# Kernel optimization log

Hardware: AMD Instinct MI355X
Metric: run time of the kernel (lower is better)

The kernel has to match this reference:

```python
import jax, jax.numpy as jnp
import numpy as np

N_NODES = 10000
N_EDGES = 160000
MUL = 128          # channel multiplicity
N_SPECIES = 10
SH_OFF = [0, 1, 4, 9, 16]   # spherical-harmonic offsets for l=0..3 (2l+1 each)
RADIAL_IN = 8
SIN_DIM = 32
MAX_DENSITY = 100.0


def setup_inputs() -> dict:
    key = jax.random.key(0)
    ks = jax.random.split(key, 16)
    inp = {
        'node_attrs': jax.random.normal(ks[0], (N_NODES, N_SPECIES), jnp.float32),
        'node_feats': jax.random.normal(ks[1], (N_NODES, MUL), jnp.float32),
        'edge_attrs': jax.random.normal(ks[2], (N_EDGES, 16), jnp.float32),
        'edge_feats': jax.random.normal(ks[3], (N_EDGES, RADIAL_IN), jnp.float32),
        'edge_index': jax.random.randint(ks[4], (2, N_EDGES), 0, N_NODES, jnp.int64),
        'W_up': jax.random.normal(ks[5], (MUL, MUL), jnp.float32),
        'Wr1': jax.random.normal(ks[6], (RADIAL_IN, 64), jnp.float32),
        'Wr2': jax.random.normal(ks[7], (64, 64), jnp.float32),
        'Wr3': jax.random.normal(ks[8], (64, 64), jnp.float32),
        'Wr4': jax.random.normal(ks[9], (64, 4 * MUL), jnp.float32),
        'Wd': jax.random.normal(ks[10], (RADIAL_IN, 1), jnp.float32),
        'Wsin': jax.random.normal(ks[11], (SIN_DIM, MUL), jnp.float32),
        'Wlin': jax.random.normal(ks[12], (4, MUL, MUL), jnp.float32),
        'Wskip': jax.random.normal(ks[13], (4, MUL, N_SPECIES, MUL), jnp.float32),
    }
    return inp


def _sinusoidal_embedding(x):
    # continuous sinusoidal embedding: dim=32, max_density=100
    half = SIN_DIM // 2
    freqs = jnp.exp(-jnp.log(MAX_DENSITY) * jnp.arange(half, dtype=x.dtype) / half)
    ang = x[:, None] * freqs[None, :]          # [N, 16]
    return jnp.concatenate([jnp.sin(ang), jnp.cos(ang)], axis=-1)  # [N, 32]


def reference(node_attrs, node_feats, edge_attrs, edge_feats, edge_index,
              W_up, Wr1, Wr2, Wr3, Wr4, Wd, Wsin, Wlin, Wskip):
    N = node_feats.shape[0]
    sender, receiver = edge_index[0], edge_index[1]

    # linear_up (e3nn o3.Linear on 128x0e, fan-in normalized)
    x = node_feats @ (W_up / np.float32(np.sqrt(MUL)))          # [N, 128]

    # radial MLP: FullyConnectedNet([8,64,64,64,512], silu), fan-in normalized
    h = edge_feats
    for W in (Wr1, Wr2, Wr3):
        h = jax.nn.silu(h @ (W / np.float32(np.sqrt(W.shape[0]))))
    tp_w = (h @ (Wr4 / np.float32(np.sqrt(64)))).reshape(-1, 4, MUL)  # [E, 4, 128]

    # equivariant TP: scalar node feats (x) gathered by sender, uvu path per SH l
    xs = x[sender]                                              # [E, 128]
    weighted = xs[:, None, :] * tp_w                            # [E, 4, 128]
    blocks = []
    for l in range(4):
        sh_l = edge_attrs[:, SH_OFF[l]:SH_OFF[l + 1]]           # [E, 2l+1]
        blk = weighted[:, l, :, None] * sh_l[:, None, :]        # [E, 128, 2l+1]
        blocks.append(blk.reshape(blk.shape[0], -1))
    mji = jnp.concatenate(blocks, axis=-1)                      # [E, 2048]

    # per-edge density gate
    density = jnp.tanh((edge_feats @ Wd) ** 2)                  # [E, 1]

    # scatter-sum messages and density to receivers
    message = jax.ops.segment_sum(mji, receiver, num_segments=N)        # [N, 2048]
    rho = jax.ops.segment_sum(density, receiver, num_segments=N)       # [N, 1]
    message = message / (rho + 1.0)

    # density embedding injected into the l=0 block
    demb = _sinusoidal_embedding(rho[:, 0]) @ Wsin              # [N, 128]
    message = message.at[:, :MUL].add(demb)

    # per-l linear (irreps_mid -> irreps_out), skip_tp with node_attrs, reshape
    out_blocks = []
    for l in range(4):
        d = 2 * l + 1
        blk = message[:, MUL * SH_OFF[l]:MUL * SH_OFF[l + 1]].reshape(N, MUL, d)
        blk = jnp.einsum('nuk,uv->nvk', blk, Wlin[l]) / np.float32(np.sqrt(MUL))
        blk = jnp.einsum('nvk,na,vaw->nwk', blk, node_attrs, Wskip[l]) \
              / np.float32(np.sqrt(MUL * N_SPECIES))
        out_blocks.append(blk)
    return jnp.concatenate(out_blocks, axis=-1)                 # [N, 128, 16]
```

## Files before the change

kernel.cpp:

```cpp
#include <hip/hip_runtime.h>
#include <hip/hip_bf16.h>

#define N_NODES 10000
#define N_EDGES 160000

typedef _Float16 h8 __attribute__((ext_vector_type(8)));
typedef _Float16 h4 __attribute__((ext_vector_type(4)));
typedef float f32x4 __attribute__((ext_vector_type(4)));

__device__ __forceinline__ float silu_f(float v){ return v / (1.f + expf(-v)); }

__global__ __launch_bounds__(256) void k_pre(const float* __restrict__ Wr2,
                                             const float* __restrict__ Wr3,
                                             const float* __restrict__ Wr4,
                                             const float* __restrict__ Wup,
                                             const float* __restrict__ Wlin,
                                             const float* __restrict__ Wskip,
                                             const int* __restrict__ eidx,
                                             _Float16* __restrict__ Wr2T,
                                             _Float16* __restrict__ Wr3T,
                                             _Float16* __restrict__ Wr4T,
                                             _Float16* __restrict__ WupT,
                                             _Float16* __restrict__ WC16T,
                                             int* __restrict__ cnt){
  const int b = blockIdx.x;
  __shared__ float wl[128];
  if (b < 224){
    const int idx = b*256 + threadIdx.x;
    if (idx < 4096){
      const int n = idx >> 6, k = idx & 63;
      Wr2T[idx] = (_Float16)(Wr2[k*64 + n] * 0.125f);
    } else if (idx < 8192){
      const int j = idx - 4096;
      const int n = j >> 6, k = j & 63;
      Wr3T[j] = (_Float16)(Wr3[k*64 + n] * 0.125f);
    } else if (idx < 40960){
      const int j = idx - 8192;
      const int n = j >> 6, k = j & 63;
      Wr4T[j] = (_Float16)(Wr4[k*512 + n] * 0.125f);
    } else if (idx < 57344){
      const int j = idx - 40960;
      const int u = j >> 7, k = j & 127;
      WupT[j] = (_Float16)(Wup[k*128 + u] * 0.08838834764831843f);
    }
  } else if (b < 736){
    const int lu = b - 224;
    const int l  = lu >> 7, u = lu & 127;
    if (threadIdx.x < 128) wl[threadIdx.x] = Wlin[lu*128 + threadIdx.x];
    __syncthreads();
    const float* Wsk = Wskip + (size_t)l * 163840;
    for (int i = threadIdx.x; i < 1280; i += 256){
      float acc = 0.f;
      #pragma unroll 16
      for (int v = 0; v < 128; ++v) acc += wl[v] * Wsk[v*1280 + i];
      const int a = i >> 7, w = i & 127;
      WC16T[((size_t)l*128 + w)*1280 + a*128 + u] =
          (_Float16)(acc * 0.0024705294220065465f);
    }
  } else {
    const int e = (b - 736)*256 + threadIdx.x;
    if (e < N_EDGES) atomicAdd(&cnt[eidx[N_EDGES + e]], 1);
  }
}

__global__ __launch_bounds__(256) void k_scan(const int* __restrict__ cnt,
                                              int* __restrict__ off,
                                              int* __restrict__ cur){
  __shared__ int sums[256];
  const int t = threadIdx.x;
  const int base = t * 40;
  int s = 0;
  for (int i = 0; i < 40; ++i){
    const int idx = base + i;
    if (idx < N_NODES) s += cnt[idx];
  }
  sums[t] = s;
  __syncthreads();
  for (int st = 1; st < 256; st <<= 1){
    const int v = (t >= st) ? sums[t - st] : 0;
    __syncthreads();
    sums[t] += v;
    __syncthreads();
  }
  int pre = (t > 0) ? sums[t - 1] : 0;
  for (int i = 0; i < 40; ++i){
    const int idx = base + i;
    if (idx < N_NODES){
      off[idx] = pre; cur[idx] = pre;
      pre += cnt[idx];
    }
  }
  if (t == 255) off[N_NODES] = sums[255];
}

__global__ __launch_bounds__(256) void k_mid(const int* __restrict__ eidx,
                                             int* __restrict__ cur,
                                             int* __restrict__ elist,
                                             int* __restrict__ esnd,
                                             const float* __restrict__ nf,
                                             const _Float16* __restrict__ WupT,
                                             float* __restrict__ x){
  const int b = blockIdx.x;
  const int tid = threadIdx.x;
  alignas(16) __shared__ _Float16 s_nf[64*128];
  alignas(16) __shared__ _Float16 s_wt[128*128];

  if (b < 625){
    const int e = b * 256 + tid;
    if (e < N_EDGES){
      const int pos = atomicAdd(&cur[eidx[N_EDGES + e]], 1);
      elist[pos] = e;
      esnd[pos]  = eidx[e];
    }
    return;
  }

  const int n0 = (b - 625) * 64;
  {
    const int rl = tid >> 2, part = tid & 3;
    const int gr = n0 + rl;
    #pragma unroll
    for (int j = 0; j < 4; ++j){
      const int cu = part*4 + j;
      h8 hv = (h8){};
      if (gr < N_NODES){
        const float4 v0 = *(const float4*)(nf + (size_t)gr*128 + cu*8);
        const float4 v1 = *(const float4*)(nf + (size_t)gr*128 + cu*8 + 4);
        hv[0]=(_Float16)v0.x; hv[1]=(_Float16)v0.y; hv[2]=(_Float16)v0.z; hv[3]=(_Float16)v0.w;
        hv[4]=(_Float16)v1.x; hv[5]=(_Float16)v1.y; hv[6]=(_Float16)v1.z; hv[7]=(_Float16)v1.w;
      }
      const int cs = (cu & 8) | ((cu & 7) ^ (rl & 7));
      *(h8*)&s_nf[rl*128 + cs*8] = hv;
    }
  }
  {
    const int rl = tid >> 1, part = tid & 1;
    #pragma unroll
    for (int j = 0; j < 8; ++j){
      const int cu = part*8 + j;
      const h8 v = *(const h8*)&WupT[(size_t)rl*128 + cu*8];
      const int cs = (cu & 8) | ((cu & 7) ^ (rl & 7));
      *(h8*)&s_wt[rl*128 + cs*8] = v;
    }
  }
  __syncthreads();

  const int wid = tid >> 6, lane = tid & 63;
  const int li = lane & 15, kg = lane >> 4;

  f32x4 acc[8];
  #pragma unroll
  for (int i = 0; i < 8; ++i) acc[i] = (f32x4){0,0,0,0};

  const int row = wid*16 + li;
  #pragma unroll
  for (int s = 0; s < 4; ++s){
    const int ca = s*4 + kg;
    const int csA = (ca & 8) | ((ca & 7) ^ (row & 7));
    const h8 af = *(const h8*)&s_nf[row*128 + csA*8];
    #pragma unroll
    for (int nt = 0; nt < 8; ++nt){
      const int u = nt*16 + li;
      const int csB = (ca & 8) | ((ca & 7) ^ (u & 7));
      const h8 bf = *(const h8*)&s_wt[u*128 + csB*8];
      acc[nt] = __builtin_amdgcn_mfma_f32_16x16x32_f16(af, bf, acc[nt], 0, 0, 0);
    }
  }
  #pragma unroll
  for (int nt = 0; nt < 8; ++nt){
    #pragma unroll
    for (int r = 0; r < 4; ++r){
      const int gr = n0 + wid*16 + kg*4 + r;
      if (gr < N_NODES) x[(size_t)gr*128 + nt*16 + li] = acc[nt][r];
    }
  }
}

__global__ __launch_bounds__(256) void k_fused(const float* __restrict__ ef,
                                               const float* __restrict__ ea,
                                               const float* __restrict__ x,
                                               const float* __restrict__ Wr1,
                                               const float* __restrict__ Wd,
                                               const _Float16* __restrict__ Wr2T,
                                               const _Float16* __restrict__ Wr3T,
                                               const _Float16* __restrict__ Wr4T,
                                               const float* __restrict__ Wsin,
                                               const int* __restrict__ off,
                                               const int* __restrict__ elist,
                                               const int* __restrict__ esnd,
                                               _Float16* __restrict__ msg16){
  const int n0 = blockIdx.x * 4;
  const int tid = threadIdx.x;
  const int lane = tid & 63, wid = tid >> 6;
  const int li = lane & 15, kg = lane >> 4;
  const int u = tid & 127, h = tid >> 7;

  __shared__ int   s_eid[32];
  __shared__ float s_ef[32][8];
  __shared__ float s_w1[8][64];
  alignas(16) __shared__ _Float16 s_xs[32][136];
  alignas(16) __shared__ _Float16 s_actA[32][64];
  alignas(16) __shared__ _Float16 s_actB[32][64];
  alignas(16) __shared__ _Float16 s_w2[32][520];
  alignas(16) __shared__ float s_sh[32][16];
  __shared__ float s_dd[32];
  __shared__ float s_rho[4];
  __shared__ int   s_offs[5];
  __shared__ float s_emb[4][32];

  if (tid < 5) s_offs[tid] = off[n0 + tid];
  if (tid < 4) s_rho[tid] = 0.f;
  for (int j = tid; j < 512; j += 256) s_w1[j >> 6][j & 63] = Wr1[j];
  __syncthreads();

  const int beg = s_offs[0], end = s_offs[4];
  const int ngrp = (end - beg + 31) >> 5;

  float a0[8] = {0,0,0,0,0,0,0,0};
  float a1[8] = {0,0,0,0,0,0,0,0};
  float a2[8] = {0,0,0,0,0,0,0,0};
  float a3[8] = {0,0,0,0,0,0,0,0};

  for (int grp = 0; grp < ngrp; ++grp){
    const int pbase = beg + grp*32;

    if (tid < 32) s_eid[tid] = (pbase + tid < end) ? elist[pbase + tid] : -1;
    __syncthreads();

    {
      const int e = tid >> 3, i = tid & 7;
      const int eid = s_eid[e];
      s_ef[e][i] = (eid >= 0) ? ef[(size_t)eid*8 + i] : 0.f;
    }
    {
      const int e = tid >> 3, qq = tid & 7;
      const int p = pbase + e;
      const int snd = (p < end) ? esnd[p] : 0;
      const float4* xp = (const float4*)(x + (size_t)snd*128 + qq*16);
      #pragma unroll
      for (int j = 0; j < 4; ++j){
        const float4 v = xp[j];
        h4 hv; hv[0]=(_Float16)v.x; hv[1]=(_Float16)v.y; hv[2]=(_Float16)v.z; hv[3]=(_Float16)v.w;
        *(h4*)&s_xs[e][qq*16 + j*4] = hv;
      }
    }
    #pragma unroll
    for (int c2 = 0; c2 < 2; ++c2){
      const int idx = c2*256 + tid;
      const int slot = idx >> 4, jj = idx & 15;
      const int eid = s_eid[slot];
      s_sh[slot][jj] = (eid >= 0) ? ea[(size_t)eid*16 + jj] : 0.f;
    }
    __syncthreads();

    if (tid < 32){
      float s = 0.f;
      #pragma unroll
      for (int i = 0; i < 8; ++i) s += s_ef[tid][i] * Wd[i];
      s_dd[tid] = tanhf(s*s);
    }

    {
      const int e = tid >> 3, ng = tid & 7;
      float hv[8] = {0,0,0,0,0,0,0,0};
      #pragma unroll
      for (int k = 0; k < 8; ++k){
        const float ev = s_ef[e][k] * 0.3535533905932738f;
        #pragma unroll
        for (int j = 0; j < 8; ++j) hv[j] += ev * s_w1[k][ng*8 + j];
      }
      h8 o;
      #pragma unroll
      for (int j = 0; j < 8; ++j) o[j] = (_Float16)silu_f(hv[j]);
      *(h8*)&s_actA[e][(ng ^ (e & 7))*8] = o;
    }
    __syncthreads();

    {
      h8 af[2];
      #pragma unroll
      for (int s = 0; s < 2; ++s)
        af[s] = *(const h8*)&Wr2T[(size_t)(wid*16 + li)*64 + s*32 + kg*8];
      #pragma unroll
      for (int nt = 0; nt < 2; ++nt){
        const int e = nt*16 + li;
        f32x4 acc = (f32x4){0,0,0,0};
        #pragma unroll
        for (int s = 0; s < 2; ++s){
          const h8 bf = *(const h8*)&s_actA[e][((s*4 + kg) ^ (e & 7))*8];
          acc = __builtin_amdgcn_mfma_f32_16x16x32_f16(af[s], bf, acc, 0, 0, 0);
        }
        #pragma unroll
        for (int r = 0; r < 4; ++r){
          const int n = wid*16 + kg*4 + r;
          s_actB[e][((n >> 3) ^ (e & 7))*8 + (n & 7)] = (_Float16)silu_f(acc[r]);
        }
      }
    }
    __syncthreads();

    {
      h8 af[2];
      #pragma unroll
      for (int s = 0; s < 2; ++s)
        af[s] = *(const h8*)&Wr3T[(size_t)(wid*16 + li)*64 + s*32 + kg*8];
      #pragma unroll
      for (int nt = 0; nt < 2; ++nt){
        const int e = nt*16 + li;
        f32x4 acc = (f32x4){0,0,0,0};
        #pragma unroll
        for (int s = 0; s < 2; ++s){
          const h8 bf = *(const h8*)&s_actB[e][((s*4 + kg) ^ (e & 7))*8];
          acc = __builtin_amdgcn_mfma_f32_16x16x32_f16(af[s], bf, acc, 0, 0, 0);
        }
        #pragma unroll
        for (int r = 0; r < 4; ++r){
          const int n = wid*16 + kg*4 + r;
          s_actA[e][((n >> 3) ^ (e & 7))*8 + (n & 7)] = (_Float16)silu_f(acc[r]);
        }
      }
    }
    __syncthreads();

    {
      h8 bf[2][2];
      #pragma unroll
      for (int nt = 0; nt < 2; ++nt){
        const int e = nt*16 + li;
        #pragma unroll
        for (int s = 0; s < 2; ++s)
          bf[nt][s] = *(const h8*)&s_actA[e][((s*4 + kg) ^ (e & 7))*8];
      }
      #pragma unroll
      for (int p = 0; p < 2; ++p){
        #pragma unroll
        for (int mt = 0; mt < 4; ++mt){
          const int nbase = wid*128 + p*64 + mt*16;
          h8 af[2];
          #pragma unroll
          for (int s = 0; s < 2; ++s)
            af[s] = *(const h8*)&Wr4T[(size_t)(nbase + li)*64 + s*32 + kg*8];
          f32x4 acc[2];
          #pragma unroll
          for (int nt = 0; nt < 2; ++nt){
            acc[nt] = (f32x4){0,0,0,0};
            #pragma unroll
            for (int s = 0; s < 2; ++s)
              acc[nt] = __builtin_amdgcn_mfma_f32_16x16x32_f16(af[s], bf[nt][s], acc[nt], 0, 0, 0);
          }
          const int c0 = nbase + kg*4;
          const int u0 = c0 & 127;
          #pragma unroll
          for (int nt = 0; nt < 2; ++nt){
            const int e = nt*16 + li;
            const h4 xv = *(const h4*)&s_xs[e][u0];
            h4 ov;
            #pragma unroll
            for (int r = 0; r < 4; ++r) ov[r] = (_Float16)acc[nt][r] * xv[r];
            *(h4*)&s_w2[e][c0] = ov;
          }
        }
      }
    }
    __syncthreads();

    int lo0 = s_offs[0] - pbase; lo0 = lo0 < 0 ? 0 : lo0;
    int hi0 = s_offs[1] - pbase; hi0 = hi0 > 32 ? 32 : (hi0 < 0 ? 0 : hi0);
    int lo1 = s_offs[1] - pbase; lo1 = lo1 < 0 ? 0 : lo1;
    int hi1 = s_offs[2] - pbase; hi1 = hi1 > 32 ? 32 : (hi1 < 0 ? 0 : hi1);
    int lo2 = s_offs[2] - pbase; lo2 = lo2 < 0 ? 0 : lo2;
    int hi2 = s_offs[3] - pbase; hi2 = hi2 > 32 ? 32 : (hi2 < 0 ? 0 : hi2);
    int lo3 = s_offs[3] - pbase; lo3 = lo3 < 0 ? 0 : lo3;
    int hi3 = s_offs[4] - pbase; hi3 = hi3 > 32 ? 32 : (hi3 < 0 ? 0 : hi3);

#define ACC_H0(A, LO, HI)                                            \
    for (int s = (LO); s < (HI); ++s){                               \
      const float wa  = (float)s_w2[s][u];                           \
      const float wb  = (float)s_w2[s][128 + u];                     \
      const float wcv = (float)s_w2[s][256 + u];                     \
      const float4 sa = *(const float4*)&s_sh[s][0];                 \
      const float4 sb = *(const float4*)&s_sh[s][4];                 \
      A[0] += wa*sa.x;                                               \
      A[1] += wb*sa.y;  A[2] += wb*sa.z;  A[3] += wb*sa.w;           \
      A[4] += wcv*sb.x; A[5] += wcv*sb.y;                            \
      A[6] += wcv*sb.z; A[7] += wcv*sb.w;                            \
    }
#define ACC_H1(A, LO, HI)                                            \
    for (int s = (LO); s < (HI); ++s){                               \
      const float wcv = (float)s_w2[s][256 + u];                     \
      const float wd  = (float)s_w2[s][384 + u];                     \
      const float4 sa = *(const float4*)&s_sh[s][8];                 \
      const float4 sb = *(const float4*)&s_sh[s][12];                \
      A[0] += wcv*sa.x;                                              \
      A[1] += wd*sa.y;  A[2] += wd*sa.z;  A[3] += wd*sa.w;           \
      A[4] += wd*sb.x;  A[5] += wd*sb.y;                             \
      A[6] += wd*sb.z;  A[7] += wd*sb.w;                             \
    }

    if (h == 0){
      ACC_H0(a0, lo0, hi0) ACC_H0(a1, lo1, hi1)
      ACC_H0(a2, lo2, hi2) ACC_H0(a3, lo3, hi3)
    } else {
      ACC_H1(a0, lo0, hi0) ACC_H1(a1, lo1, hi1)
      ACC_H1(a2, lo2, hi2) ACC_H1(a3, lo3, hi3)
    }

    if (tid < 4){
      int lo = s_offs[tid]     - pbase; lo = lo < 0 ? 0 : lo;
      int hi = s_offs[tid + 1] - pbase; hi = hi > 32 ? 32 : (hi < 0 ? 0 : hi);
      float r = 0.f;
      for (int s = lo; s < hi; ++s) r += s_dd[s];
      s_rho[tid] += r;
    }
    __syncthreads();
  }

  if (tid < 64){
    const int ni = tid >> 4, f = tid & 15;
    const float fr  = expf(-0.28782313662425572f * (float)f);
    const float ang = s_rho[ni] * fr;
    s_emb[ni][f]      = sinf(ang);
    s_emb[ni][f + 16] = cosf(ang);
  }
  __syncthreads();

  float db0 = 0.f, db1 = 0.f, db2 = 0.f, db3 = 0.f;
  if (h == 0){
    #pragma unroll 8
    for (int j = 0; j < 32; ++j){
      const float wsv = Wsin[j*128 + u];
      db0 += s_emb[0][j]*wsv; db1 += s_emb[1][j]*wsv;
      db2 += s_emb[2][j]*wsv; db3 += s_emb[3][j]*wsv;
    }
  }
  const float t0 = 1.f/(s_rho[0]+1.f), t1 = 1.f/(s_rho[1]+1.f);
  const float t2 = 1.f/(s_rho[2]+1.f), t3 = 1.f/(s_rho[3]+1.f);
  #pragma unroll
  for (int j = 0; j < 8; ++j){
    float v0 = a0[j]*t0, v1 = a1[j]*t1, v2 = a2[j]*t2, v3 = a3[j]*t3;
    if (h == 0 && j == 0){ v0 += db0; v1 += db1; v2 += db2; v3 += db3; }
    const size_t base = (size_t)(h*8 + j)*128 + u;
    msg16[(size_t)(n0+0)*2048 + base] = (_Float16)v0;
    msg16[(size_t)(n0+1)*2048 + base] = (_Float16)v1;
    msg16[(size_t)(n0+2)*2048 + base] = (_Float16)v2;
    msg16[(size_t)(n0+3)*2048 + base] = (_Float16)v3;
  }
}

template<int L, int D>
__device__ __forceinline__ void final_body(const int bb,
                                           const _Float16* __restrict__ msg16,
                                           const float* __restrict__ attrs,
                                           const _Float16* __restrict__ WC16T,
                                           float* __restrict__ outD,
                                           _Float16* __restrict__ sA,
                                           _Float16* __restrict__ sB,
                                           _Float16* __restrict__ sAttr){
  constexpr int OFF  = (L==0 ? 0 : L==1 ? 1 : L==2 ? 4 : 9);
  constexpr int ROWS = N_NODES * D;
  const int r0  = bb * 128;
  const int tid = threadIdx.x;

  {
    const int rl = tid >> 2, quarter = tid & 3;
    const int gr = r0 + rl;
    h8 vals[4];
    if (gr < ROWS){
      const int n = gr / D, k = gr - n*D;
      const _Float16* src = msg16 + (size_t)n*2048 + (size_t)(OFF+k)*128 + quarter*32;
      #pragma unroll
      for (int j = 0; j < 4; ++j) vals[j] = *(const h8*)(src + j*8);
    } else {
      #pragma unroll
      for (int j = 0; j < 4; ++j) vals[j] = (h8){};
    }
    #pragma unroll
    for (int j = 0; j < 4; ++j){
      const int cu = quarter*4 + j;
      const int cs = (cu & 8) | ((cu & 7) ^ (rl & 7));
      *(h8*)&sA[rl*128 + cs*8] = vals[j];
    }
  }
  for (int i = tid; i < 1280; i += 512){
    const int rl = i / 10, aa = i - rl*10;
    const int gr = r0 + rl;
    sAttr[i] = (gr < ROWS) ? (_Float16)attrs[(gr / D)*10 + aa] : (_Float16)0.f;
  }
  {
    const int w = tid >> 2, part = tid & 3;
    const _Float16* src = WC16T + ((size_t)L*128 + w)*1280 + part*16;
    #pragma unroll
    for (int j = 0; j < 2; ++j){
      const h8 v = *(const h8*)(src + j*8);
      const int cc = part*2 + j;
      *(h8*)&sB[w*64 + (cc ^ (w & 7))*8] = v;
    }
  }
  __syncthreads();

  const int wid = tid >> 6, lane = tid & 63;
  const int wm = wid >> 2, wn = wid & 3;
  const int li = lane & 15, kg = lane >> 4;

  f32x4 acc[4][2];
  #pragma unroll
  for (int m = 0; m < 4; ++m)
    #pragma unroll
    for (int nn = 0; nn < 2; ++nn) acc[m][nn] = (f32x4){0,0,0,0};

  for (int step = 0; step < 20; ++step){
    _Float16* sbc = (step & 1) ? (sB + 8192) : sB;
    _Float16* sbn = (step & 1) ? sB : (sB + 8192);
    const bool more = (step + 1 < 20);
    h8 pre[2];
    if (more){
      const int a2 = (step+1) >> 1, u02 = ((step+1) & 1) << 6;
      const _Float16* src = WC16T + ((size_t)L*128 + (tid>>2))*1280 + a2*128 + u02 + (tid&3)*16;
      #pragma unroll
      for (int j = 0; j < 2; ++j) pre[j] = *(const h8*)(src + j*8);
    }

    const int a  = step >> 1;
    const int uh = (step & 1) << 3;

    h8 afr[4][2], bfr[2][2];
    #pragma unroll
    for (int m = 0; m < 4; ++m){
      const int row = wm*64 + m*16 + li;
      const _Float16 av = sAttr[row*10 + a];
      h8 avx;
      #pragma unroll
      for (int j = 0; j < 8; ++j) avx[j] = av;
      #pragma unroll
      for (int s = 0; s < 2; ++s){
        const int ca = uh + s*4 + kg;
        const int cs = (ca & 8) | ((ca & 7) ^ (row & 7));
        const h8 mA = *(const h8*)&sA[row*128 + cs*8];
        afr[m][s] = mA * avx;
      }
    }
    #pragma unroll
    for (int nn = 0; nn < 2; ++nn){
      const int w = wn*32 + nn*16 + li;
      #pragma unroll
      for (int s = 0; s < 2; ++s){
        const int cb = s*4 + kg;
        bfr[nn][s] = *(const h8*)&sbc[w*64 + ((cb ^ (w & 7)))*8];
      }
    }
    #pragma unroll
    for (int s = 0; s < 2; ++s)
      #pragma unroll
      for (int m = 0; m < 4; ++m)
        #pragma unroll
        for (int nn = 0; nn < 2; ++nn)
          acc[m][nn] = __builtin_amdgcn_mfma_f32_16x16x32_f16(afr[m][s], bfr[nn][s], acc[m][nn], 0, 0, 0);

    if (more){
      const int w = tid >> 2, part = tid & 3;
      #pragma unroll
      for (int j = 0; j < 2; ++j){
        const int cc = part*2 + j;
        *(h8*)&sbn[w*64 + (cc ^ (w & 7))*8] = pre[j];
      }
    }
    __syncthreads();
  }

  #pragma unroll
  for (int m = 0; m < 4; ++m){
    const int rbase = r0 + wm*64 + m*16 + kg*4;
    #pragma unroll
    for (int rr = 0; rr < 4; ++rr){
      const int gr = rbase + rr;
      if (gr < ROWS){
        float* op = outD + (size_t)gr*128;
        #pragma unroll
        for (int nn = 0; nn < 2; ++nn)
          op[wn*32 + nn*16 + li] = acc[m][nn][rr];
      }
    }
  }
}

__global__ __launch_bounds__(512) void k_final_all(const _Float16* __restrict__ msg16,
                                                   const float* __restrict__ attrs,
                                                   const _Float16* __restrict__ WC16T,
                                                   float* __restrict__ outD){
  alignas(16) __shared__ _Float16 sA[128*128];
  alignas(16) __shared__ _Float16 sB[2*64*128];
  __shared__ _Float16 sAttr[128*10];
  const int b = blockIdx.x;
  if (b < 79)       final_body<0,1>(b,       msg16, attrs, WC16T, outD,            sA, sB, sAttr);
  else if (b < 314) final_body<1,3>(b - 79,  msg16, attrs, WC16T, outD + 1280000,  sA, sB, sAttr);
  else if (b < 705) final_body<2,5>(b - 314, msg16, attrs, WC16T, outD + 5120000,  sA, sB, sAttr);
  else              final_body<3,7>(b - 705, msg16, attrs, WC16T, outD + 11520000, sA, sB, sAttr);
}

__global__ __launch_bounds__(256) void k_merge(const float* __restrict__ outD,
                                               float* __restrict__ out){
  const int n0 = blockIdx.x * 4;
  const int tid = threadIdx.x;
  __shared__ float lds[4*16*132];

  {
    const float4* src = (const float4*)(outD + (size_t)n0*128);
    for (int j = tid; j < 128; j += 256){
      const int row = j >> 5, c4 = j & 31;
      *(float4*)&lds[(row*16 + 0)*132 + c4*4] = src[j];
    }
  }
  {
    const float4* src = (const float4*)(outD + 1280000 + (size_t)n0*3*128);
    for (int j = tid; j < 384; j += 256){
      const int row = j >> 5, c4 = j & 31;
      const int nloc = row/3, k = row - nloc*3;
      *(float4*)&lds[(nloc*16 + 1 + k)*132 + c4*4] = src[j];
    }
  }
  {
    const float4* src = (const float4*)(outD + 5120000 + (size_t)n0*5*128);
    for (int j = tid; j < 640; j += 256){
      const int row = j >> 5, c4 = j & 31;
      const int nloc = row/5, k = row - nloc*5;
      *(float4*)&lds[(nloc*16 + 4 + k)*132 + c4*4] = src[j];
    }
  }
  {
    const float4* src = (const float4*)(outD + 11520000 + (size_t)n0*7*128);
    for (int j = tid; j < 896; j += 256){
      const int row = j >> 5, c4 = j & 31;
      const int nloc = row/7, k = row - nloc*7;
      *(float4*)&lds[(nloc*16 + 9 + k)*132 + c4*4] = src[j];
    }
  }
  __syncthreads();

  for (int j = tid; j < 2048; j += 256){
    const int nloc = j >> 9, qv = j & 511;
    const int w = qv >> 2, s0 = (qv & 3) << 2;
    float4 v;
    v.x = lds[(nloc*16 + s0 + 0)*132 + w];
    v.y = lds[(nloc*16 + s0 + 1)*132 + w];
    v.z = lds[(nloc*16 + s0 + 2)*132 + w];
    v.w = lds[(nloc*16 + s0 + 3)*132 + w];
    *(float4*)&out[(size_t)(n0 + nloc)*2048 + qv*4] = v;
  }
}

extern "C" void kernel_launch(void* const* d_in, const int* in_sizes, int n_in,
                              void* d_out, int out_size, void* d_ws, size_t ws_size,
                              hipStream_t stream){
  const float* node_attrs = (const float*)d_in[0];
  const float* node_feats = (const float*)d_in[1];
  const float* edge_attrs = (const float*)d_in[2];
  const float* edge_feats = (const float*)d_in[3];
  const int*   edge_index = (const int*)d_in[4];
  const float* W_up  = (const float*)d_in[5];
  const float* Wr1   = (const float*)d_in[6];
  const float* Wr2   = (const float*)d_in[7];
  const float* Wr3   = (const float*)d_in[8];
  const float* Wr4   = (const float*)d_in[9];
  const float* Wd    = (const float*)d_in[10];
  const float* Wsin  = (const float*)d_in[11];
  const float* Wlin  = (const float*)d_in[12];
  const float* Wskip = (const float*)d_in[13];
  float* out = (float*)d_out;

  float* outD     = (float*)d_ws;
  _Float16* msg16 = (_Float16*)(outD + 20480000);
  float* x        = (float*)(msg16 + 20480000);
  _Float16* WC16T = (_Float16*)(x + 1280000);
  int* cnt   = (int*)(WC16T + 655360);
  int* off   = cnt + 10000;
  int* cur   = off + 10016;
  int* elist = cur + 10000;
  int* esnd  = elist + 160000;
  _Float16* Wr2T = (_Float16*)(esnd + 160000);
  _Float16* Wr3T = Wr2T + 4096;
  _Float16* Wr4T = Wr3T + 4096;
  _Float16* WupT = Wr4T + 32768;

  hipMemsetAsync(cnt, 0, (size_t)10000 * sizeof(int), stream);

  k_pre<<<1361, 256, 0, stream>>>(Wr2, Wr3, Wr4, W_up, Wlin, Wskip, edge_index,
                                  Wr2T, Wr3T, Wr4T, WupT, WC16T, cnt);
  k_scan<<<1, 256, 0, stream>>>(cnt, off, cur);
  k_mid<<<782, 256, 0, stream>>>(edge_index, cur, elist, esnd,
                                 node_feats, WupT, x);

  k_fused<<<N_NODES/4, 256, 0, stream>>>(edge_feats, edge_attrs, x,
                                         Wr1, Wd, Wr2T, Wr3T, Wr4T, Wsin,
                                         off, elist, esnd, msg16);

  k_final_all<<<1252, 512, 0, stream>>>(msg16, node_attrs, WC16T, outD);

  k_merge<<<2500, 256, 0, stream>>>(outD, out);
}
```

Before: 319.3 us.

## Pre-permute edge data into receiver order and double-buffer edge loads in fused kernel

During the CSR bucketing pass, edge features and edge attributes are now copied into receiver-sorted arrays, so the indirect elist lookup disappears and the fused kernel reads contiguous data. The fused kernel also double-buffers its shared-memory tiles (edge features, spherical harmonics, sender features): the next group's loads are issued into registers while the current group computes, then written to the other buffer. This cuts dependent-load latency and one barrier per group, at the cost of extra scattered writes in k_mid, more workspace, and higher register and shared-memory use.

```diff
diff --git a/kernel.cpp b/kernel.cpp
--- a/kernel.cpp
+++ b/kernel.cpp
@@ -94,9 +94,12 @@
 }
 
 __global__ __launch_bounds__(256) void k_mid(const int* __restrict__ eidx,
+                                             const float* __restrict__ ef,
+                                             const float* __restrict__ ea,
                                              int* __restrict__ cur,
-                                             int* __restrict__ elist,
                                              int* __restrict__ esnd,
+                                             float* __restrict__ efp,
+                                             float* __restrict__ eap,
                                              const float* __restrict__ nf,
                                              const _Float16* __restrict__ WupT,
                                              float* __restrict__ x){
@@ -109,8 +112,13 @@
     const int e = b * 256 + tid;
     if (e < N_EDGES){
       const int pos = atomicAdd(&cur[eidx[N_EDGES + e]], 1);
-      elist[pos] = e;
-      esnd[pos]  = eidx[e];
+      esnd[pos] = eidx[e];
+      const float4* efs = (const float4*)(ef + (size_t)e*8);
+      float4* efd = (float4*)(efp + (size_t)pos*8);
+      efd[0] = efs[0]; efd[1] = efs[1];
+      const float4* eas = (const float4*)(ea + (size_t)e*16);
+      float4* ead = (float4*)(eap + (size_t)pos*16);
+      ead[0] = eas[0]; ead[1] = eas[1]; ead[2] = eas[2]; ead[3] = eas[3];
     }
     return;
   }
@@ -176,8 +184,8 @@
   }
 }
 
-__global__ __launch_bounds__(256) void k_fused(const float* __restrict__ ef,
-                                               const float* __restrict__ ea,
+__global__ __launch_bounds__(256) void k_fused(const float* __restrict__ efp,
+                                               const float* __restrict__ eap,
                                                const float* __restrict__ x,
                                                const float* __restrict__ Wr1,
                                                const float* __restrict__ Wd,
@@ -186,7 +194,6 @@
                                                const _Float16* __restrict__ Wr4T,
                                                const float* __restrict__ Wsin,
                                                const int* __restrict__ off,
-                                               const int* __restrict__ elist,
                                                const int* __restrict__ esnd,
                                                _Float16* __restrict__ msg16){
   const int n0 = blockIdx.x * 4;
@@ -195,14 +202,13 @@
   const int li = lane & 15, kg = lane >> 4;
   const int u = tid & 127, h = tid >> 7;
 
-  __shared__ int   s_eid[32];
-  __shared__ float s_ef[32][8];
+  __shared__ float s_ef[2][32][8];
   __shared__ float s_w1[8][64];
-  alignas(16) __shared__ _Float16 s_xs[32][136];
+  alignas(16) __shared__ _Float16 s_xs[2][32][132];
   alignas(16) __shared__ _Float16 s_actA[32][64];
   alignas(16) __shared__ _Float16 s_actB[32][64];
   alignas(16) __shared__ _Float16 s_w2[32][520];
-  alignas(16) __shared__ float s_sh[32][16];
+  alignas(16) __shared__ float s_sh[2][32][16];
   __shared__ float s_dd[32];
   __shared__ float s_rho[4];
   __shared__ int   s_offs[5];
@@ -216,47 +222,50 @@
   const int beg = s_offs[0], end = s_offs[4];
   const int ngrp = (end - beg + 31) >> 5;
 
+  const int e8 = tid >> 3, i8 = tid & 7;
+  const int slotB = tid >> 4, jjB = tid & 15;
+
   float a0[8] = {0,0,0,0,0,0,0,0};
   float a1[8] = {0,0,0,0,0,0,0,0};
   float a2[8] = {0,0,0,0,0,0,0,0};
   float a3[8] = {0,0,0,0,0,0,0,0};
 
-  for (int grp = 0; grp < ngrp; ++grp){
-    const int pbase = beg + grp*32;
-
-    if (tid < 32) s_eid[tid] = (pbase + tid < end) ? elist[pbase + tid] : -1;
-    __syncthreads();
-
-    {
-      const int e = tid >> 3, i = tid & 7;
-      const int eid = s_eid[e];
-      s_ef[e][i] = (eid >= 0) ? ef[(size_t)eid*8 + i] : 0.f;
-    }
-    {
-      const int e = tid >> 3, qq = tid & 7;
-      const int p = pbase + e;
-      const int snd = (p < end) ? esnd[p] : 0;
-      const float4* xp = (const float4*)(x + (size_t)snd*128 + qq*16);
-      #pragma unroll
-      for (int j = 0; j < 4; ++j){
-        const float4 v = xp[j];
-        h4 hv; hv[0]=(_Float16)v.x; hv[1]=(_Float16)v.y; hv[2]=(_Float16)v.z; hv[3]=(_Float16)v.w;
-        *(h4*)&s_xs[e][qq*16 + j*4] = hv;
-      }
-    }
-    #pragma unroll
-    for (int c2 = 0; c2 < 2; ++c2){
-      const int idx = c2*256 + tid;
-      const int slot = idx >> 4, jj = idx & 15;
-      const int eid = s_eid[slot];
-      s_sh[slot][jj] = (eid >= 0) ? ea[(size_t)eid*16 + jj] : 0.f;
-    }
-    __syncthreads();
+  if (ngrp > 0){
+    const int p = beg + e8;
+    s_ef[0][e8][i8] = (p < end) ? efp[(size_t)p*8 + i8] : 0.f;
+    const int pB0 = beg + slotB, pB1 = beg + slotB + 16;
+    s_sh[0][slotB][jjB]      = (pB0 < end) ? eap[(size_t)pB0*16 + jjB] : 0.f;
+    s_sh[0][slotB + 16][jjB] = (pB1 < end) ? eap[(size_t)pB1*16 + jjB] : 0.f;
+    const int snd = (p < end) ? esnd[p] : 0;
+    const float4* xp = (const float4*)(x + (size_t)snd*128 + i8*16);
+    #pragma unroll
+    for (int j = 0; j < 4; ++j){
+      const float4 v = xp[j];
+      h4 hv; hv[0]=(_Float16)v.x; hv[1]=(_Float16)v.y; hv[2]=(_Float16)v.z; hv[3]=(_Float16)v.w;
+      *(h4*)&s_xs[0][e8][i8*16 + j*4] = hv;
+    }
+  }
+  __syncthreads();
+
+  for (int g = 0; g < ngrp; ++g){
+    const int cur = g & 1, nxt = cur ^ 1;
+    const int pbase  = beg + g*32;
+    const int pbase2 = pbase + 32;
+    const bool more = (g + 1 < ngrp);
+
+    float ef_r = 0.f, sh_r0 = 0.f, sh_r1 = 0.f;
+    int snd_r = 0;
+    const int pA = pbase2 + e8;
+    const bool vA = more && (pA < end);
+    if (vA){ ef_r = efp[(size_t)pA*8 + i8]; snd_r = esnd[pA]; }
+    const int pB0 = pbase2 + slotB, pB1 = pbase2 + slotB + 16;
+    if (more && pB0 < end) sh_r0 = eap[(size_t)pB0*16 + jjB];
+    if (more && pB1 < end) sh_r1 = eap[(size_t)pB1*16 + jjB];
 
     if (tid < 32){
       float s = 0.f;
       #pragma unroll
-      for (int i = 0; i < 8; ++i) s += s_ef[tid][i] * Wd[i];
+      for (int i = 0; i < 8; ++i) s += s_ef[cur][tid][i] * Wd[i];
       s_dd[tid] = tanhf(s*s);
     }
 
@@ -265,7 +274,7 @@
       float hv[8] = {0,0,0,0,0,0,0,0};
       #pragma unroll
       for (int k = 0; k < 8; ++k){
-        const float ev = s_ef[e][k] * 0.3535533905932738f;
+        const float ev = s_ef[cur][e][k] * 0.3535533905932738f;
         #pragma unroll
         for (int j = 0; j < 8; ++j) hv[j] += ev * s_w1[k][ng*8 + j];
       }
@@ -298,6 +307,12 @@
       }
     }
     __syncthreads();
+
+    float4 xs_r0 = {0,0,0,0}, xs_r1 = {0,0,0,0}, xs_r2 = {0,0,0,0}, xs_r3 = {0,0,0,0};
+    if (vA){
+      const float4* xp = (const float4*)(x + (size_t)snd_r*128 + i8*16);
+      xs_r0 = xp[0]; xs_r1 = xp[1]; xs_r2 = xp[2]; xs_r3 = xp[3];
+    }
 
     {
       h8 af[2];
@@ -353,7 +368,7 @@
           #pragma unroll
           for (int nt = 0; nt < 2; ++nt){
             const int e = nt*16 + li;
-            const h4 xv = *(const h4*)&s_xs[e][u0];
+            const h4 xv = *(const h4*)&s_xs[cur][e][u0];
             h4 ov;
             #pragma unroll
             for (int r = 0; r < 4; ++r) ov[r] = (_Float16)acc[nt][r] * xv[r];
@@ -378,8 +393,8 @@
       const float wa  = (float)s_w2[s][u];                           \
       const float wb  = (float)s_w2[s][128 + u];                     \
       const float wcv = (float)s_w2[s][256 + u];                     \
-      const float4 sa = *(const float4*)&s_sh[s][0];                 \
-      const float4 sb = *(const float4*)&s_sh[s][4];                 \
+      const float4 sa = *(const float4*)&s_sh[cur][s][0];            \
+      const float4 sb = *(const float4*)&s_sh[cur][s][4];            \
       A[0] += wa*sa.x;                                               \
       A[1] += wb*sa.y;  A[2] += wb*sa.z;  A[3] += wb*sa.w;           \
       A[4] += wcv*sb.x; A[5] += wcv*sb.y;                            \
@@ -389,8 +404,8 @@
     for (int s = (LO); s < (HI); ++s){                               \
       const float wcv = (float)s_w2[s][256 + u];                     \
       const float wd  = (float)s_w2[s][384 + u];                     \
-      const float4 sa = *(const float4*)&s_sh[s][8];                 \
-      const float4 sb = *(const float4*)&s_sh[s][12];                \
+      const float4 sa = *(const float4*)&s_sh[cur][s][8];            \
+      const float4 sb = *(const float4*)&s_sh[cur][s][12];           \
       A[0] += wcv*sa.x;                                              \
       A[1] += wd*sa.y;  A[2] += wd*sa.z;  A[3] += wd*sa.w;           \
       A[4] += wd*sb.x;  A[5] += wd*sb.y;                             \
@@ -411,6 +426,19 @@
       float r = 0.f;
       for (int s = lo; s < hi; ++s) r += s_dd[s];
       s_rho[tid] += r;
+    }
+
+    if (more){
+      s_ef[nxt][e8][i8] = ef_r;
+      s_sh[nxt][slotB][jjB]      = sh_r0;
+      s_sh[nxt][slotB + 16][jjB] = sh_r1;
+      const float4 xr[4] = {xs_r0, xs_r1, xs_r2, xs_r3};
+      #pragma unroll
+      for (int j = 0; j < 4; ++j){
+        h4 hv; hv[0]=(_Float16)xr[j].x; hv[1]=(_Float16)xr[j].y;
+        hv[2]=(_Float16)xr[j].z; hv[3]=(_Float16)xr[j].w;
+        *(h4*)&s_xs[nxt][e8][i8*16 + j*4] = hv;
+      }
     }
     __syncthreads();
   }
@@ -674,9 +702,10 @@
   int* cnt   = (int*)(WC16T + 655360);
   int* off   = cnt + 10000;
   int* cur   = off + 10016;
-  int* elist = cur + 10000;
-  int* esnd  = elist + 160000;
-  _Float16* Wr2T = (_Float16*)(esnd + 160000);
+  int* esnd  = cur + 10000;
+  float* efp = (float*)(esnd + 160000);
+  float* eap = efp + 1280000;
+  _Float16* Wr2T = (_Float16*)(eap + 2560000);
   _Float16* Wr3T = Wr2T + 4096;
   _Float16* Wr4T = Wr3T + 4096;
   _Float16* WupT = Wr4T + 32768;
@@ -686,12 +715,13 @@
   k_pre<<<1361, 256, 0, stream>>>(Wr2, Wr3, Wr4, W_up, Wlin, Wskip, edge_index,
                                   Wr2T, Wr3T, Wr4T, WupT, WC16T, cnt);
   k_scan<<<1, 256, 0, stream>>>(cnt, off, cur);
-  k_mid<<<782, 256, 0, stream>>>(edge_index, cur, elist, esnd,
+  k_mid<<<782, 256, 0, stream>>>(edge_index, edge_feats, edge_attrs,
+                                 cur, esnd, efp, eap,
                                  node_feats, WupT, x);
 
-  k_fused<<<N_NODES/4, 256, 0, stream>>>(edge_feats, edge_attrs, x,
+  k_fused<<<N_NODES/4, 256, 0, stream>>>(efp, eap, x,
                                          Wr1, Wd, Wr2T, Wr3T, Wr4T, Wsin,
-                                         off, elist, esnd, msg16);
+                                         off, esnd, msg16);
 
   k_final_all<<<1252, 512, 0, stream>>>(msg16, node_attrs, WC16T, outD);
 
```

Result: faster. 310.6 us (-2.7%).
